# Kernel tuning notes

Measured on AMD Instinct MI355X. Metric: run time of the kernel, lower is better.

## Reference

```python
import jax, jax.numpy as jnp
import numpy as np

HEADS = 16


def setup_inputs() -> dict:
    key = jax.random.key(0)
    ks = jax.random.split(key, 7)
    B, N, MEM, DIM = 2, 2048, 2048, 1024
    J = MEM + N
    x = jax.random.normal(ks[0], (B, N, DIM), dtype=jnp.float32)
    mem = jax.random.normal(ks[1], (B, MEM, DIM), dtype=jnp.float32)
    expire_mask = jax.random.uniform(ks[2], (B, 1, 1, J), dtype=jnp.float32)
    Wq = jax.random.normal(ks[3], (DIM, DIM), dtype=jnp.float32) * 0.02
    Wkv = jax.random.normal(ks[4], (DIM, 2 * DIM), dtype=jnp.float32) * 0.02
    Wo = jax.random.normal(ks[5], (DIM, DIM), dtype=jnp.float32) * 0.02
    bo = jnp.zeros((DIM,), dtype=jnp.float32)
    return {"x": x, "mem": mem, "expire_mask": expire_mask,
            "Wq": Wq, "Wkv": Wkv, "Wo": Wo, "bo": bo}


def reference(x, mem, expire_mask, Wq, Wkv, Wo, bo):
    b, n, dim = x.shape
    h = HEADS
    d = dim // h
    scale = d ** -0.5
    mem_len = mem.shape[1]

    q = x @ Wq                                   # [b, n, dim]
    context = jnp.concatenate([mem, x], axis=1)  # [b, j, dim]
    kv = context @ Wkv                           # [b, j, 2*dim]
    k, v = jnp.split(kv, 2, axis=-1)

    def to_heads(t):
        bb, nn, _ = t.shape
        return t.reshape(bb, nn, h, d).transpose(0, 2, 1, 3)  # b h n d

    q, k, v = map(to_heads, (q, k, v))

    dots = jnp.einsum('bhid,bhjd->bhij', q, k) * scale  # [b,h,n,j]
    j_len = dots.shape[-1]
    # causal mask with memory offset: position i attends to j <= i + mem_len
    i_idx = jnp.arange(n)[:, None]
    j_idx = jnp.arange(j_len)[None, :]
    causal = j_idx > (i_idx + mem_len)           # True => masked
    dots = jnp.where(causal[None, None], -jnp.inf, dots)

    attn = jax.nn.softmax(dots, axis=-1)
    attn = attn * expire_mask                    # post-softmax expire gating

    out = jnp.einsum('bhij,bhjd->bhid', attn, v)  # [b,h,n,d]
    out = out.transpose(0, 2, 1, 3).reshape(b, n, dim)
    return out @ Wo + bo
```

## Files before the change

kernel.cpp:

```cpp
#include <hip/hip_runtime.h>
#include <cstdint>

typedef __bf16 bf16_t;
typedef __attribute__((ext_vector_type(2))) __bf16 bf16x2;
typedef __attribute__((ext_vector_type(4))) __bf16 bf16x4;
typedef __attribute__((ext_vector_type(8))) __bf16 bf16x8;
typedef __attribute__((ext_vector_type(4))) float f32x4;
typedef __attribute__((ext_vector_type(16))) float f32x16;
typedef __attribute__((ext_vector_type(4))) int i32x4;

constexpr int Bx = 2, Nx = 2048, MEMx = 2048, Jx = 4096, DIMx = 1024, Hx = 16, HDx = 64;

__device__ __forceinline__ void gload_lds16(const bf16_t* g, bf16_t* lds) {
  __builtin_amdgcn_global_load_lds(
      (const __attribute__((address_space(1))) unsigned int*)g,
      (__attribute__((address_space(3))) unsigned int*)lds, 16, 0, 0);
}

__device__ __forceinline__ int pk2(float a, float b) {
  bf16x2 t;
  t[0] = (bf16_t)a;
  t[1] = (bf16_t)b;
  return __builtin_bit_cast(int, t);
}

__device__ __forceinline__ void pl32swap(int& a, int& b) {
  asm volatile("v_permlane32_swap_b32 %0, %1" : "+v"(a), "+v"(b));
}

__global__ void k_build_bf16(const float* __restrict__ x, const float* __restrict__ mem,
                             bf16_t* __restrict__ xb, bf16_t* __restrict__ ctxb) {
  const int XT = Bx * Nx * DIMx;
  const int CT = Bx * Jx * DIMx;
  for (int i = blockIdx.x * blockDim.x + threadIdx.x; i < XT + CT;
       i += gridDim.x * blockDim.x) {
    if (i < XT) {
      xb[i] = (bf16_t)x[i];
    } else {
      int c = i - XT;
      int bb = c / (Jx * DIMx);
      int rr = c % (Jx * DIMx);
      int j = rr / DIMx, d = rr % DIMx;
      float v = (j < MEMx) ? mem[(int64_t)(bb * MEMx + j) * DIMx + d]
                           : x[(int64_t)(bb * Nx + (j - MEMx)) * DIMx + d];
      ctxb[c] = (bf16_t)v;
    }
  }
}

__global__ void k_transpose_w(const float* __restrict__ W, bf16_t* __restrict__ WT,
                              int K, int Nc) {
  int total = K * Nc;
  for (int i = blockIdx.x * blockDim.x + threadIdx.x; i < total;
       i += gridDim.x * blockDim.x) {
    int n = i / K, k = i % K;
    WT[i] = (bf16_t)W[(int64_t)k * Nc + n];
  }
}

template <int OUTF32>
__launch_bounds__(256)
__global__ void k_gemm_bt(const bf16_t* __restrict__ A, const bf16_t* __restrict__ BT,
                          void* __restrict__ Cv, const float* __restrict__ bias,
                          const float* __restrict__ gate, int gate_col0, float scale,
                          int M, int Nc, int K) {
  __shared__ bf16_t As[2][128 * 32];
  __shared__ bf16_t Bs[2][128 * 32];
  const int tid = threadIdx.x;
  const int w = tid >> 6, l = tid & 63;
  const int lr = l & 15, lg = l >> 4;
  const int m0 = blockIdx.y * 128, n0 = blockIdx.x * 128;
  const int wm = (w >> 1) * 64, wn = (w & 1) * 64;

  const int srow = w * 16 + (l >> 2);
  const int scol = (l & 3) * 8;
  const bf16_t* ga0 = A + (int64_t)(m0 + srow) * K + scol;
  const bf16_t* gb0 = BT + (int64_t)(n0 + srow) * K + scol;

  auto stage = [&](int bufi, int k0) {
    bf16_t* lA = &As[bufi][0] + w * 512;
    bf16_t* lB = &Bs[bufi][0] + w * 512;
    gload_lds16(ga0 + k0, lA);
    gload_lds16(ga0 + (int64_t)64 * K + k0, lA + 2048);
    gload_lds16(gb0 + k0, lB);
    gload_lds16(gb0 + (int64_t)64 * K + k0, lB + 2048);
  };

  f32x4 acc[4][4] = {};

  stage(0, 0);
  __syncthreads();

  const int nsteps = K >> 5;
  for (int t = 0; t < nsteps; ++t) {
    const int cur = t & 1;
    if (t + 1 < nsteps) stage(cur ^ 1, (t + 1) << 5);

    bf16x8 af[4], bfr[4];
#pragma unroll
    for (int q = 0; q < 4; ++q)
      af[q] = *(const bf16x8*)(&As[cur][0] + (wm + q * 16 + lr) * 32 + lg * 8);
#pragma unroll
    for (int q = 0; q < 4; ++q)
      bfr[q] = *(const bf16x8*)(&Bs[cur][0] + (wn + q * 16 + lr) * 32 + lg * 8);
#pragma unroll
    for (int mt = 0; mt < 4; ++mt)
#pragma unroll
      for (int nt = 0; nt < 4; ++nt)
        acc[mt][nt] = __builtin_amdgcn_mfma_f32_16x16x32_bf16(af[mt], bfr[nt],
                                                              acc[mt][nt], 0, 0, 0);
    __syncthreads();
  }

#pragma unroll
  for (int mt = 0; mt < 4; ++mt) {
#pragma unroll
    for (int nt = 0; nt < 4; ++nt) {
      int col = n0 + wn + nt * 16 + lr;
#pragma unroll
      for (int r = 0; r < 4; ++r) {
        int row = m0 + wm + mt * 16 + lg * 4 + r;
        float v = acc[mt][nt][r] * scale;
        if (gate != nullptr && col >= gate_col0) v *= gate[row];
        if constexpr (OUTF32) {
          ((float*)Cv)[(int64_t)row * Nc + col] = v + bias[col];
        } else {
          ((bf16_t*)Cv)[(int64_t)row * Nc + col] = (bf16_t)v;
        }
      }
    }
  }
}

__launch_bounds__(256)
__global__ void k_attn(const bf16_t* __restrict__ Q, const bf16_t* __restrict__ KV,
                       bf16_t* __restrict__ Hout) {
  __shared__ bf16_t Ks[2][64 * 64];
  __shared__ bf16_t Vs[2][64 * 80];

  const int tid = threadIdx.x;
  const int w = tid >> 6, l = tid & 63;
  const int ql = l & 31, hi = l >> 5;
  const int b = blockIdx.z, h = blockIdx.y;
  const int qi = b ? (gridDim.x - 1 - blockIdx.x) : blockIdx.x;
  const int q0 = qi * 128;

  const bf16_t* Qb = Q + ((int64_t)b * Nx) * DIMx + h * HDx;
  const bf16_t* Kb = KV + ((int64_t)b * Jx) * (2 * DIMx) + h * HDx;
  const bf16_t* Vb = Kb + DIMx;

  const int qrow = q0 + w * 32 + ql;

  bf16x8 qf[4];
#pragma unroll
  for (int dt = 0; dt < 4; ++dt)
    qf[dt] = *(const bf16x8*)(Qb + (int64_t)qrow * DIMx + dt * 16 + hi * 8);

  int koff[2][4], voff[2][4];
#pragma unroll
  for (int jb = 0; jb < 2; ++jb)
#pragma unroll
    for (int dt = 0; dt < 4; ++dt)
      koff[jb][dt] = (jb * 32 + ql) * 128 + (((dt * 2 + hi) * 16) ^ ((ql & 7) * 16));
#pragma unroll
  for (int db = 0; db < 2; ++db)
#pragma unroll
    for (int jt = 0; jt < 4; ++jt)
      voff[db][jt] = (db * 32 + ql) * 160 +
                     (((jt * 2 + hi) * 16) ^ (((db * 4 + (ql >> 3)) & 7) * 16));

  f32x16 o[2] = {};
  float mrun = -1e30f, lsum = 0.f;

  const int ksrow = w * 16 + (l >> 3);
  const int kscol = ((l & 7) ^ (l >> 3)) * 8;
  const int jend = (Jx < q0 + 128 + MEMx) ? Jx : (q0 + 128 + MEMx);
  const int nt_tiles = jend >> 6;
  const f32x16 z16 = {};

  const bf16_t* vsrc0 = Vb + (int64_t)(w * 8 + (l >> 3)) * 2048 + (l & 7) * 8;
  const int vd0 = (l & 7) * 8;
  const int vrow2 = (l >> 3) * 2;
  const int chx0 = ((w) ^ (l & 7)) * 16;
  const int chx1 = ((4 + w) ^ (l & 7)) * 16;

  auto stageK = [&](int bufi, int j0) {
    bf16_t* kd = &Ks[bufi][0] + w * 1024;
    const bf16_t* src = Kb + (int64_t)(j0 + ksrow) * 2048 + kscol;
    gload_lds16(src, kd);
    gload_lds16(src + (int64_t)8 * 2048, kd + 512);
  };
  auto loadV = [&](int j0, bf16x8& a, bf16x8& c) {
    const bf16_t* s = vsrc0 + (int64_t)j0 * 2048;
    a = *(const bf16x8*)s;
    c = *(const bf16x8*)(s + (int64_t)32 * 2048);
  };
  auto writeV = [&](int bufi, bf16x8 a, bf16x8 c) {
    char* base = (char*)&Vs[bufi][0];
#pragma unroll
    for (int i = 0; i < 8; ++i)
      *(bf16_t*)(base + (vd0 + i) * 160 + chx0 + vrow2) = a[i];
#pragma unroll
    for (int i = 0; i < 8; ++i)
      *(bf16_t*)(base + (vd0 + i) * 160 + chx1 + vrow2) = c[i];
  };

  bf16x8 vA, vC;
  stageK(0, 0);
  loadV(0, vA, vC);
  writeV(0, vA, vC);
  __syncthreads();

  for (int t = 0; t < nt_tiles; ++t) {
    const int cur = t & 1;
    const int j0 = t << 6;
    const bool pf = (t + 1 < nt_tiles);
    if (pf) {
      stageK(cur ^ 1, j0 + 64);
      loadV(j0 + 64, vA, vC);
    }
    const char* KsC = (const char*)&Ks[cur][0];
    const char* VsC = (const char*)&Vs[cur][0];

    f32x16 s[2];
    __builtin_amdgcn_s_setprio(1);
#pragma unroll
    for (int jb = 0; jb < 2; ++jb) {
      f32x16 acc = z16;
#pragma unroll
      for (int dt = 0; dt < 4; ++dt) {
        bf16x8 kf = *(const bf16x8*)(KsC + koff[jb][dt]);
        acc = __builtin_amdgcn_mfma_f32_32x32x16_bf16(kf, qf[dt], acc, 0, 0, 0);
      }
      s[jb] = acc;
    }
    __builtin_amdgcn_s_setprio(0);

    if (j0 + 63 > q0 + MEMx) {
#pragma unroll
      for (int jb = 0; jb < 2; ++jb)
#pragma unroll
        for (int r = 0; r < 16; ++r) {
          int j = j0 + jb * 32 + (r & 3) + (r >> 2) * 8 + hi * 4;
          if (j > qrow + MEMx) s[jb][r] = -1e30f;
        }
    }

    f32x16 tv = __builtin_elementwise_max(s[0], s[1]);
    float t8[8], t4[4];
#pragma unroll
    for (int i = 0; i < 8; ++i) t8[i] = fmaxf(tv[i], tv[i + 8]);
#pragma unroll
    for (int i = 0; i < 4; ++i) t4[i] = fmaxf(t8[i], t8[i + 4]);
    float tm = fmaxf(fmaxf(t4[0], t4[1]), fmaxf(t4[2], t4[3]));
    tm = fmaxf(tm, __shfl_xor(tm, 32));

    if (!__all(tm <= mrun + 8.f)) {
      float mnew = fmaxf(mrun, tm);
      float al = exp2f(mrun - mnew);
      mrun = mnew;
      lsum *= al;
#pragma unroll
      for (int db = 0; db < 2; ++db)
#pragma unroll
        for (int r = 0; r < 16; ++r) o[db][r] *= al;
    }

#pragma unroll
    for (int jb = 0; jb < 2; ++jb)
#pragma unroll
      for (int r = 0; r < 16; ++r) s[jb][r] = exp2f(s[jb][r] - mrun);

    f32x16 av = s[0] + s[1];
    float a8[8], a4[4];
#pragma unroll
    for (int i = 0; i < 8; ++i) a8[i] = av[i] + av[i + 8];
#pragma unroll
    for (int i = 0; i < 4; ++i) a4[i] = a8[i] + a8[i + 4];
    float ps = (a4[0] + a4[1]) + (a4[2] + a4[3]);
    ps += __shfl_xor(ps, 32);
    lsum += ps;

    bf16x8 pfrag[4];
#pragma unroll
    for (int jb = 0; jb < 2; ++jb) {
      int pw[8];
#pragma unroll
      for (int g = 0; g < 8; ++g) pw[g] = pk2(s[jb][2 * g], s[jb][2 * g + 1]);
      pl32swap(pw[0], pw[2]);
      pl32swap(pw[1], pw[3]);
      pl32swap(pw[4], pw[6]);
      pl32swap(pw[5], pw[7]);
      i32x4 f0 = {pw[0], pw[1], pw[2], pw[3]};
      i32x4 f1 = {pw[4], pw[5], pw[6], pw[7]};
      pfrag[jb * 2] = __builtin_bit_cast(bf16x8, f0);
      pfrag[jb * 2 + 1] = __builtin_bit_cast(bf16x8, f1);
    }

    __builtin_amdgcn_s_setprio(1);
#pragma unroll
    for (int db = 0; db < 2; ++db)
#pragma unroll
      for (int jt = 0; jt < 4; ++jt) {
        bf16x8 vf = *(const bf16x8*)(VsC + voff[db][jt]);
        o[db] = __builtin_amdgcn_mfma_f32_32x32x16_bf16(vf, pfrag[jt], o[db], 0, 0, 0);
      }
    __builtin_amdgcn_s_setprio(0);

    if (pf) writeV(cur ^ 1, vA, vC);
    __syncthreads();
  }

  float inv = 1.f / lsum;
#pragma unroll
  for (int db = 0; db < 2; ++db)
#pragma unroll
    for (int g = 0; g < 4; ++g) {
      bf16x4 ov;
#pragma unroll
      for (int r = 0; r < 4; ++r) ov[r] = (bf16_t)(o[db][g * 4 + r] * inv);
      *(bf16x4*)(Hout + (int64_t)(b * Nx + qrow) * DIMx + h * HDx + db * 32 + g * 8 +
                 hi * 4) = ov;
    }
}

extern "C" void kernel_launch(void* const* d_in, const int* in_sizes, int n_in,
                              void* d_out, int out_size, void* d_ws, size_t ws_size,
                              hipStream_t stream) {
  const float* x    = (const float*)d_in[0];
  const float* mem  = (const float*)d_in[1];
  const float* expm = (const float*)d_in[2];
  const float* Wq   = (const float*)d_in[3];
  const float* Wkv  = (const float*)d_in[4];
  const float* Wo   = (const float*)d_in[5];
  const float* bo   = (const float*)d_in[6];
  float* out = (float*)d_out;

  bf16_t* p = (bf16_t*)d_ws;
  bf16_t* xb   = p; p += (size_t)Bx * Nx * DIMx;
  bf16_t* ctxb = p; p += (size_t)Bx * Jx * DIMx;
  bf16_t* WqT  = p; p += (size_t)DIMx * DIMx;
  bf16_t* WkvT = p; p += (size_t)DIMx * 2 * DIMx;
  bf16_t* WoT  = p; p += (size_t)DIMx * DIMx;
  bf16_t* Qb   = p; p += (size_t)Bx * Nx * DIMx;
  bf16_t* KVb  = p; p += (size_t)Bx * Jx * 2 * DIMx;
  bf16_t* Ho   = p; p += (size_t)Bx * Nx * DIMx;

  k_build_bf16<<<4096, 256, 0, stream>>>(x, mem, xb, ctxb);
  k_transpose_w<<<1024, 256, 0, stream>>>(Wq, WqT, DIMx, DIMx);
  k_transpose_w<<<2048, 256, 0, stream>>>(Wkv, WkvT, DIMx, 2 * DIMx);
  k_transpose_w<<<1024, 256, 0, stream>>>(Wo, WoT, DIMx, DIMx);

  const float qscale = 0.125f * 1.4426950408889634f;
  k_gemm_bt<0><<<dim3(1024 / 128, 4096 / 128), 256, 0, stream>>>(
      xb, WqT, Qb, nullptr, nullptr, 0x7fffffff, qscale, Bx * Nx, DIMx, DIMx);
  k_gemm_bt<0><<<dim3(2048 / 128, 8192 / 128), 256, 0, stream>>>(
      ctxb, WkvT, KVb, nullptr, expm, DIMx, 1.0f, Bx * Jx, 2 * DIMx, DIMx);
  k_attn<<<dim3(Nx / 128, Hx, Bx), 256, 0, stream>>>(Qb, KVb, Ho);
  k_gemm_bt<1><<<dim3(1024 / 128, 4096 / 128), 256, 0, stream>>>(
      Ho, WoT, out, bo, nullptr, 0x7fffffff, 1.0f, Bx * Nx, DIMx, DIMx);
}
```

Baseline: 302.0 us.

## Split attention key range into two chunks and merge with combine kernel

Each attention block now handles one of two key-range halves (memory part and causal part), doubling the grid to 1024 blocks. Each block writes unnormalized partial outputs plus running max and sum, and a new combine kernel rescales and merges them. The aim is better load balance and occupancy across CUs, since causal work per query tile varies. In exchange it adds extra global traffic for partial outputs, an extra launch, and bf16 rounding of unnormalized partials. The row-max reduction also switches to v_max3 instructions.

```diff
diff --git a/kernel.cpp b/kernel.cpp
--- a/kernel.cpp
+++ b/kernel.cpp
@@ -26,6 +26,12 @@
 
 __device__ __forceinline__ void pl32swap(int& a, int& b) {
   asm volatile("v_permlane32_swap_b32 %0, %1" : "+v"(a), "+v"(b));
+}
+
+__device__ __forceinline__ float fmax3(float a, float b, float c) {
+  float d;
+  asm("v_max3_f32 %0, %1, %2, %3" : "=v"(d) : "v"(a), "v"(b), "v"(c));
+  return d;
 }
 
 __global__ void k_build_bf16(const float* __restrict__ x, const float* __restrict__ mem,
@@ -134,15 +140,18 @@
 
 __launch_bounds__(256)
 __global__ void k_attn(const bf16_t* __restrict__ Q, const bf16_t* __restrict__ KV,
-                       bf16_t* __restrict__ Hout) {
+                       bf16_t* __restrict__ Opart, float2* __restrict__ ML) {
   __shared__ bf16_t Ks[2][64 * 64];
   __shared__ bf16_t Vs[2][64 * 80];
 
   const int tid = threadIdx.x;
   const int w = tid >> 6, l = tid & 63;
   const int ql = l & 31, hi = l >> 5;
-  const int b = blockIdx.z, h = blockIdx.y;
-  const int qi = b ? (gridDim.x - 1 - blockIdx.x) : blockIdx.x;
+
+  const int lin = blockIdx.x;
+  const int qi0 = lin & 15, h = (lin >> 4) & 15;
+  const int c = (lin >> 8) & 1, b = lin >> 9;
+  const int qi = b ? (15 - qi0) : qi0;
   const int q0 = qi * 128;
 
   const bf16_t* Qb = Q + ((int64_t)b * Nx) * DIMx + h * HDx;
@@ -174,8 +183,9 @@
 
   const int ksrow = w * 16 + (l >> 3);
   const int kscol = ((l & 7) ^ (l >> 3)) * 8;
-  const int jend = (Jx < q0 + 128 + MEMx) ? Jx : (q0 + 128 + MEMx);
-  const int nt_tiles = jend >> 6;
+  const int jstart = c * 2048;
+  const int jend = c ? ((Jx < q0 + 128 + MEMx) ? Jx : (q0 + 128 + MEMx)) : 2048;
+  const int nt_tiles = (jend - jstart) >> 6;
   const f32x16 z16 = {};
 
   const bf16_t* vsrc0 = Vb + (int64_t)(w * 8 + (l >> 3)) * 2048 + (l & 7) * 8;
@@ -190,30 +200,30 @@
     gload_lds16(src, kd);
     gload_lds16(src + (int64_t)8 * 2048, kd + 512);
   };
-  auto loadV = [&](int j0, bf16x8& a, bf16x8& c) {
+  auto loadV = [&](int j0, bf16x8& a, bf16x8& cc) {
     const bf16_t* s = vsrc0 + (int64_t)j0 * 2048;
     a = *(const bf16x8*)s;
-    c = *(const bf16x8*)(s + (int64_t)32 * 2048);
+    cc = *(const bf16x8*)(s + (int64_t)32 * 2048);
   };
-  auto writeV = [&](int bufi, bf16x8 a, bf16x8 c) {
+  auto writeV = [&](int bufi, bf16x8 a, bf16x8 cc) {
     char* base = (char*)&Vs[bufi][0];
 #pragma unroll
     for (int i = 0; i < 8; ++i)
       *(bf16_t*)(base + (vd0 + i) * 160 + chx0 + vrow2) = a[i];
 #pragma unroll
     for (int i = 0; i < 8; ++i)
-      *(bf16_t*)(base + (vd0 + i) * 160 + chx1 + vrow2) = c[i];
+      *(bf16_t*)(base + (vd0 + i) * 160 + chx1 + vrow2) = cc[i];
   };
 
   bf16x8 vA, vC;
-  stageK(0, 0);
-  loadV(0, vA, vC);
+  stageK(0, jstart);
+  loadV(jstart, vA, vC);
   writeV(0, vA, vC);
   __syncthreads();
 
   for (int t = 0; t < nt_tiles; ++t) {
     const int cur = t & 1;
-    const int j0 = t << 6;
+    const int j0 = jstart + (t << 6);
     const bool pf = (t + 1 < nt_tiles);
     if (pf) {
       stageK(cur ^ 1, j0 + 64);
@@ -246,13 +256,17 @@
         }
     }
 
-    f32x16 tv = __builtin_elementwise_max(s[0], s[1]);
-    float t8[8], t4[4];
-#pragma unroll
-    for (int i = 0; i < 8; ++i) t8[i] = fmaxf(tv[i], tv[i + 8]);
-#pragma unroll
-    for (int i = 0; i < 4; ++i) t4[i] = fmaxf(t8[i], t8[i + 4]);
-    float tm = fmaxf(fmaxf(t4[0], t4[1]), fmaxf(t4[2], t4[3]));
+    float t12[12];
+#pragma unroll
+    for (int i = 0; i < 10; ++i)
+      t12[i] = fmax3(s[(3 * i) >> 4][(3 * i) & 15], s[(3 * i + 1) >> 4][(3 * i + 1) & 15],
+                     s[(3 * i + 2) >> 4][(3 * i + 2) & 15]);
+    t12[10] = s[1][14];
+    t12[11] = s[1][15];
+    float t4[4];
+#pragma unroll
+    for (int i = 0; i < 4; ++i) t4[i] = fmax3(t12[3 * i], t12[3 * i + 1], t12[3 * i + 2]);
+    float tm = fmaxf(fmax3(t4[0], t4[1], t4[2]), t4[3]);
     tm = fmaxf(tm, __shfl_xor(tm, 32));
 
     if (!__all(tm <= mrun + 8.f)) {
@@ -311,17 +325,46 @@
     __syncthreads();
   }
 
-  float inv = 1.f / lsum;
+  bf16_t* op = Opart + (int64_t)c * (Bx * Nx * DIMx) +
+               (int64_t)(b * Nx + qrow) * DIMx + h * HDx;
 #pragma unroll
   for (int db = 0; db < 2; ++db)
 #pragma unroll
     for (int g = 0; g < 4; ++g) {
       bf16x4 ov;
 #pragma unroll
-      for (int r = 0; r < 4; ++r) ov[r] = (bf16_t)(o[db][g * 4 + r] * inv);
-      *(bf16x4*)(Hout + (int64_t)(b * Nx + qrow) * DIMx + h * HDx + db * 32 + g * 8 +
-                 hi * 4) = ov;
-    }
+      for (int r = 0; r < 4; ++r) ov[r] = (bf16_t)o[db][g * 4 + r];
+      *(bf16x4*)(op + db * 32 + g * 8 + hi * 4) = ov;
+    }
+  if (hi == 0)
+    ML[((int64_t)(c * Bx + b) * Hx + h) * Nx + qrow] = make_float2(mrun, lsum);
+}
+
+__global__ void k_combine(const bf16_t* __restrict__ Op, const float2* __restrict__ ML,
+                          bf16_t* __restrict__ Ho) {
+  const int64_t CH = (int64_t)Bx * Nx * DIMx;
+  int i = blockIdx.x * blockDim.x + threadIdx.x;
+  const int total = (int)(CH >> 3);
+  if (i >= total) return;
+  int64_t off = (int64_t)i * 8;
+  int bqh = (int)(off >> 6);
+  int h = bqh & 15;
+  int bq = bqh >> 4;
+  int b = bq >> 11, q = bq & (Nx - 1);
+  float2 ml0 = ML[((int64_t)b * Hx + h) * Nx + q];
+  float2 ml1 = ML[((int64_t)(Bx + b) * Hx + h) * Nx + q];
+  float M = fmaxf(ml0.x, ml1.x);
+  float a0 = exp2f(ml0.x - M), a1 = exp2f(ml1.x - M);
+  float inv = 1.f / (a0 * ml0.y + a1 * ml1.y);
+  a0 *= inv;
+  a1 *= inv;
+  bf16x8 v0 = *(const bf16x8*)(Op + off);
+  bf16x8 v1 = *(const bf16x8*)(Op + CH + off);
+  bf16x8 outv;
+#pragma unroll
+  for (int r = 0; r < 8; ++r)
+    outv[r] = (bf16_t)(a0 * (float)v0[r] + a1 * (float)v1[r]);
+  *(bf16x8*)(Ho + off) = outv;
 }
 
 extern "C" void kernel_launch(void* const* d_in, const int* in_sizes, int n_in,
@@ -346,6 +389,9 @@
   bf16_t* KVb  = p; p += (size_t)Bx * Jx * 2 * DIMx;
   bf16_t* Ho   = p; p += (size_t)Bx * Nx * DIMx;
 
+  bf16_t* Opart = ctxb;
+  float2* ML    = (float2*)xb;
+
   k_build_bf16<<<4096, 256, 0, stream>>>(x, mem, xb, ctxb);
   k_transpose_w<<<1024, 256, 0, stream>>>(Wq, WqT, DIMx, DIMx);
   k_transpose_w<<<2048, 256, 0, stream>>>(Wkv, WkvT, DIMx, 2 * DIMx);
@@ -356,7 +402,10 @@
       xb, WqT, Qb, nullptr, nullptr, 0x7fffffff, qscale, Bx * Nx, DIMx, DIMx);
   k_gemm_bt<0><<<dim3(2048 / 128, 8192 / 128), 256, 0, stream>>>(
       ctxb, WkvT, KVb, nullptr, expm, DIMx, 1.0f, Bx * Jx, 2 * DIMx, DIMx);
-  k_attn<<<dim3(Nx / 128, Hx, Bx), 256, 0, stream>>>(Qb, KVb, Ho);
+
+  k_attn<<<1024, 256, 0, stream>>>(Qb, KVb, Opart, ML);
+  k_combine<<<(Bx * Nx * DIMx / 8 + 255) / 256, 256, 0, stream>>>(Opart, ML, Ho);
+
   k_gemm_bt<1><<<dim3(1024 / 128, 4096 / 128), 256, 0, stream>>>(
       Ho, WoT, out, bo, nullptr, 0x7fffffff, 1.0f, Bx * Nx, DIMx, DIMx);
 }
```

Measured after the change: 301.0 us. Within noise of the previous version (-0.3%).
